# Performance work log

Hardware: AMD Instinct MI355X
Metric: run time of the kernel (lower is better)

## Reference

```python
import jax, jax.numpy as jnp
import numpy as np

S, H = 8192, 2048


def setup_inputs() -> dict:
    key = jax.random.key(0)
    k1, k2, k3, k4, k5 = jax.random.split(key, 5)
    encoder_outputs = jax.random.normal(k1, (S, 1, H), dtype=jnp.float32)
    hidden = jax.random.normal(k2, (H,), dtype=jnp.float32)
    # nn.Linear(2H, H): weight [H, 2H], bias [H]
    lim = 1.0 / np.sqrt(2 * H)
    W_att = jax.random.uniform(k3, (H, 2 * H), dtype=jnp.float32, minval=-lim, maxval=lim)
    b_att = jax.random.uniform(k4, (H,), dtype=jnp.float32, minval=-lim, maxval=lim)
    w = jax.random.normal(k5, (1, H), dtype=jnp.float32)
    return {"encoder_outputs": encoder_outputs, "hidden": hidden,
            "W_att": W_att, "b_att": b_att, "w": w}


def reference(encoder_outputs, hidden, W_att, b_att, w):
    # Original loops over source_len: score_i = w . (Linear(cat(hidden, enc_i)))
    # Vectorized: build [S, 2H] once, one GEMM, one dot, one softmax.
    enc = encoder_outputs[:, 0, :]                      # [S, H]
    h = jnp.broadcast_to(hidden[None, :], enc.shape)    # [S, H]
    x = jnp.concatenate([h, enc], axis=1)               # [S, 2H]
    res = x @ W_att.T + b_att                           # [S, H]
    scores = res @ w[0]                                 # [S]
    attn = jax.nn.softmax(scores, axis=0)               # softmax over source_len
    return attn[None, None, :]                          # [1, 1, S]
```

## Files before the change

kernel.cpp:

```cpp
#include <hip/hip_runtime.h>
#include <math.h>

#define SS 8192
#define HH 2048

__global__ void colsum_kernel(const float* __restrict__ W,
                              const float* __restrict__ w,
                              float* __restrict__ v2) {
    const int t       = threadIdx.x;
    const int colBase = blockIdx.x * 1024;
    const int row0    = blockIdx.y * 32;
    const float4* base =
        (const float4*)(W + (size_t)row0 * (2 * HH) + HH + colBase) + t;
    float4 acc = {0.f, 0.f, 0.f, 0.f};
#pragma unroll
    for (int j = 0; j < 32; ++j) {
        float4 a = base[(size_t)j * ((2 * HH) / 4)];
        float wj = w[row0 + j];
        acc.x += wj * a.x; acc.y += wj * a.y;
        acc.z += wj * a.z; acc.w += wj * a.w;
    }
    float* dst = v2 + colBase + t * 4;
    atomicAdd(dst + 0, acc.x);
    atomicAdd(dst + 1, acc.y);
    atomicAdd(dst + 2, acc.z);
    atomicAdd(dst + 3, acc.w);
}

__global__ __launch_bounds__(256) void rowdot_kernel(
    const float* __restrict__ enc,
    const float* __restrict__ v2,
    float* __restrict__ sc)
{
    const int wave = threadIdx.x >> 6;
    const int lane = threadIdx.x & 63;
    const float4* v = (const float4*)v2;
    float4 vf[8];
#pragma unroll
    for (int i = 0; i < 8; ++i) vf[i] = v[lane + i * 64];

    const int row_base = blockIdx.x * 8 + wave * 2;
#pragma unroll
    for (int rr = 0; rr < 2; ++rr) {
        const int row = row_base + rr;
        const float4* e = (const float4*)(enc + (size_t)row * HH);
        float acc = 0.0f;
#pragma unroll
        for (int i = 0; i < 8; ++i) {
            float4 a = e[lane + i * 64];
            acc += a.x * vf[i].x + a.y * vf[i].y
                 + a.z * vf[i].z + a.w * vf[i].w;
        }
#pragma unroll
        for (int off = 32; off > 0; off >>= 1)
            acc += __shfl_down(acc, off);
        if (lane == 0) sc[row] = acc;
    }
}

__global__ __launch_bounds__(256) void softmax_kernel(
    const float* __restrict__ sc,
    float* __restrict__ out)
{
    __shared__ float red[4];
    const int t    = threadIdx.x;
    const int lane = t & 63;
    const int wid  = t >> 6;

    float vals[32];
    float m = -INFINITY;
#pragma unroll
    for (int i = 0; i < 32; ++i) {
        vals[i] = sc[t + i * 256];
        m = fmaxf(m, vals[i]);
    }
#pragma unroll
    for (int off = 1; off < 64; off <<= 1)
        m = fmaxf(m, __shfl_xor(m, off));
    if (lane == 0) red[wid] = m;
    __syncthreads();
    m = fmaxf(fmaxf(red[0], red[1]), fmaxf(red[2], red[3]));

    float s = 0.0f;
#pragma unroll
    for (int i = 0; i < 32; ++i)
        s += __expf(vals[i] - m);
#pragma unroll
    for (int off = 1; off < 64; off <<= 1)
        s += __shfl_xor(s, off);
    __syncthreads();
    if (lane == 0) red[wid] = s;
    __syncthreads();
    const float inv = 1.0f / (red[0] + red[1] + red[2] + red[3]);

    if (t < 16) {
        const int e = blockIdx.x * 16 + t;
        out[e] = __expf(sc[e] - m) * inv;
    }
}

extern "C" void kernel_launch(void* const* d_in, const int* in_sizes, int n_in,
                              void* d_out, int out_size, void* d_ws, size_t ws_size,
                              hipStream_t stream) {
    const float* enc   = (const float*)d_in[0];
    const float* W_att = (const float*)d_in[2];
    const float* w     = (const float*)d_in[4];

    float* out = (float*)d_out;
    float* v2  = (float*)d_ws;
    float* sc  = v2 + HH;

    hipMemsetAsync(v2, 0, HH * sizeof(float), stream);
    hipLaunchKernelGGL(colsum_kernel,  dim3(2, 64), dim3(256), 0, stream,
                       W_att, w, v2);
    hipLaunchKernelGGL(rowdot_kernel,  dim3(1024), dim3(256), 0, stream,
                       enc, v2, sc);
    hipLaunchKernelGGL(softmax_kernel, dim3(512),  dim3(256), 0, stream,
                       sc, out);
}
```

Baseline: 126.0 us.

## Fuse colsum, rowdot and softmax into one persistent kernel with grid barriers

Replaces the memset plus three kernel launches with a single persistent kernel of 256 blocks that synchronises phases through a software grid barrier built on device-scope atomics. The w·W column-sum vector now lives in a device global, and block 0 re-zeroes it at the end so the memset is no longer needed. The aim is to remove launch gaps and inter-kernel drain. The cost is that all blocks must be co-resident for the barrier to work, and blocks spin-wait on atomics in between phases.

```diff
diff --git a/kernel.cpp b/kernel.cpp
--- a/kernel.cpp
+++ b/kernel.cpp
@@ -3,99 +3,138 @@
 
 #define SS 8192
 #define HH 2048
+#define NBLK 256
+#define NTHR 512
 
-__global__ void colsum_kernel(const float* __restrict__ W,
-                              const float* __restrict__ w,
-                              float* __restrict__ v2) {
-    const int t       = threadIdx.x;
-    const int colBase = blockIdx.x * 1024;
-    const int row0    = blockIdx.y * 32;
-    const float4* base =
-        (const float4*)(W + (size_t)row0 * (2 * HH) + HH + colBase) + t;
-    float4 acc = {0.f, 0.f, 0.f, 0.f};
-#pragma unroll
-    for (int j = 0; j < 32; ++j) {
-        float4 a = base[(size_t)j * ((2 * HH) / 4)];
-        float wj = w[row0 + j];
-        acc.x += wj * a.x; acc.y += wj * a.y;
-        acc.z += wj * a.z; acc.w += wj * a.w;
+__device__ unsigned g_count = 0;
+__device__ unsigned g_gen   = 0;
+__device__ __align__(16) float g_v2[HH];
+
+__device__ __forceinline__ void grid_barrier() {
+    __syncthreads();
+    if (threadIdx.x == 0) {
+        __threadfence();
+        unsigned my  = __hip_atomic_load(&g_gen, __ATOMIC_RELAXED,
+                                         __HIP_MEMORY_SCOPE_AGENT);
+        unsigned old = __hip_atomic_fetch_add(&g_count, 1u, __ATOMIC_ACQ_REL,
+                                              __HIP_MEMORY_SCOPE_AGENT);
+        if (old == NBLK - 1u) {
+            __hip_atomic_store(&g_count, 0u, __ATOMIC_RELAXED,
+                               __HIP_MEMORY_SCOPE_AGENT);
+            __hip_atomic_fetch_add(&g_gen, 1u, __ATOMIC_RELEASE,
+                                   __HIP_MEMORY_SCOPE_AGENT);
+        } else {
+            while (__hip_atomic_load(&g_gen, __ATOMIC_ACQUIRE,
+                                     __HIP_MEMORY_SCOPE_AGENT) == my)
+                __builtin_amdgcn_s_sleep(2);
+        }
+        __threadfence();
     }
-    float* dst = v2 + colBase + t * 4;
-    atomicAdd(dst + 0, acc.x);
-    atomicAdd(dst + 1, acc.y);
-    atomicAdd(dst + 2, acc.z);
-    atomicAdd(dst + 3, acc.w);
+    __syncthreads();
 }
 
-__global__ __launch_bounds__(256) void rowdot_kernel(
+__global__ __launch_bounds__(NTHR, 2) void fused_kernel(
     const float* __restrict__ enc,
-    const float* __restrict__ v2,
+    const float* __restrict__ W,
+    const float* __restrict__ w,
+    float* __restrict__ out,
     float* __restrict__ sc)
 {
-    const int wave = threadIdx.x >> 6;
-    const int lane = threadIdx.x & 63;
-    const float4* v = (const float4*)v2;
-    float4 vf[8];
+    const int b = blockIdx.x;
+    const int t = threadIdx.x;
+
+    {
+        const int row0 = b * 8;
+        const float4* base =
+            (const float4*)(W + (size_t)row0 * (2 * HH) + HH) + t;
+        float4 acc = {0.f, 0.f, 0.f, 0.f};
 #pragma unroll
-    for (int i = 0; i < 8; ++i) vf[i] = v[lane + i * 64];
+        for (int j = 0; j < 8; ++j) {
+            float4 a = base[(size_t)j * ((2 * HH) / 4)];
+            float wj = w[row0 + j];
+            acc.x += wj * a.x; acc.y += wj * a.y;
+            acc.z += wj * a.z; acc.w += wj * a.w;
+        }
+        float* dst = g_v2 + t * 4;
+        atomicAdd(dst + 0, acc.x);
+        atomicAdd(dst + 1, acc.y);
+        atomicAdd(dst + 2, acc.z);
+        atomicAdd(dst + 3, acc.w);
+    }
 
-    const int row_base = blockIdx.x * 8 + wave * 2;
+    grid_barrier();
+
+    {
+        const int wave = t >> 6;
+        const int lane = t & 63;
+        const float4* v = (const float4*)g_v2;
+        float4 vf[8];
 #pragma unroll
-    for (int rr = 0; rr < 2; ++rr) {
-        const int row = row_base + rr;
-        const float4* e = (const float4*)(enc + (size_t)row * HH);
-        float acc = 0.0f;
+        for (int i = 0; i < 8; ++i) vf[i] = v[lane + i * 64];
+
+        const int row_base = b * 32 + wave * 4;
 #pragma unroll
-        for (int i = 0; i < 8; ++i) {
-            float4 a = e[lane + i * 64];
-            acc += a.x * vf[i].x + a.y * vf[i].y
-                 + a.z * vf[i].z + a.w * vf[i].w;
+        for (int rr = 0; rr < 4; ++rr) {
+            const int row = row_base + rr;
+            const float4* e = (const float4*)(enc + (size_t)row * HH);
+            float acc = 0.0f;
+#pragma unroll
+            for (int i = 0; i < 8; ++i) {
+                float4 a = e[lane + i * 64];
+                acc += a.x * vf[i].x + a.y * vf[i].y
+                     + a.z * vf[i].z + a.w * vf[i].w;
+            }
+#pragma unroll
+            for (int off = 32; off > 0; off >>= 1)
+                acc += __shfl_down(acc, off);
+            if (lane == 0) sc[row] = acc;
+        }
+    }
+
+    grid_barrier();
+
+    {
+        __shared__ float red[8];
+        const int lane = t & 63;
+        const int wid  = t >> 6;
+
+        float vals[16];
+        float m = -INFINITY;
+#pragma unroll
+        for (int i = 0; i < 16; ++i) {
+            vals[i] = sc[t + i * 512];
+            m = fmaxf(m, vals[i]);
         }
 #pragma unroll
-        for (int off = 32; off > 0; off >>= 1)
-            acc += __shfl_down(acc, off);
-        if (lane == 0) sc[row] = acc;
-    }
-}
+        for (int off = 1; off < 64; off <<= 1)
+            m = fmaxf(m, __shfl_xor(m, off));
+        if (lane == 0) red[wid] = m;
+        __syncthreads();
+#pragma unroll
+        for (int k = 0; k < 8; ++k) m = fmaxf(m, red[k]);
 
-__global__ __launch_bounds__(256) void softmax_kernel(
-    const float* __restrict__ sc,
-    float* __restrict__ out)
-{
-    __shared__ float red[4];
-    const int t    = threadIdx.x;
-    const int lane = t & 63;
-    const int wid  = t >> 6;
+        float s = 0.0f;
+#pragma unroll
+        for (int i = 0; i < 16; ++i)
+            s += __expf(vals[i] - m);
+#pragma unroll
+        for (int off = 1; off < 64; off <<= 1)
+            s += __shfl_xor(s, off);
+        __syncthreads();
+        if (lane == 0) red[wid] = s;
+        __syncthreads();
+        float ss = 0.0f;
+#pragma unroll
+        for (int k = 0; k < 8; ++k) ss += red[k];
+        const float inv = 1.0f / ss;
 
-    float vals[32];
-    float m = -INFINITY;
-#pragma unroll
-    for (int i = 0; i < 32; ++i) {
-        vals[i] = sc[t + i * 256];
-        m = fmaxf(m, vals[i]);
-    }
-#pragma unroll
-    for (int off = 1; off < 64; off <<= 1)
-        m = fmaxf(m, __shfl_xor(m, off));
-    if (lane == 0) red[wid] = m;
-    __syncthreads();
-    m = fmaxf(fmaxf(red[0], red[1]), fmaxf(red[2], red[3]));
+        if (t < 32) {
+            const int e = b * 32 + t;
+            out[e] = __expf(sc[e] - m) * inv;
+        }
 
-    float s = 0.0f;
-#pragma unroll
-    for (int i = 0; i < 32; ++i)
-        s += __expf(vals[i] - m);
-#pragma unroll
-    for (int off = 1; off < 64; off <<= 1)
-        s += __shfl_xor(s, off);
-    __syncthreads();
-    if (lane == 0) red[wid] = s;
-    __syncthreads();
-    const float inv = 1.0f / (red[0] + red[1] + red[2] + red[3]);
-
-    if (t < 16) {
-        const int e = blockIdx.x * 16 + t;
-        out[e] = __expf(sc[e] - m) * inv;
+        if (b == 0)
+            ((float4*)g_v2)[t] = make_float4(0.f, 0.f, 0.f, 0.f);
     }
 }
 
@@ -107,14 +146,8 @@
     const float* w     = (const float*)d_in[4];
 
     float* out = (float*)d_out;
-    float* v2  = (float*)d_ws;
-    float* sc  = v2 + HH;
+    float* sc  = (float*)d_ws;
 
-    hipMemsetAsync(v2, 0, HH * sizeof(float), stream);
-    hipLaunchKernelGGL(colsum_kernel,  dim3(2, 64), dim3(256), 0, stream,
-                       W_att, w, v2);
-    hipLaunchKernelGGL(rowdot_kernel,  dim3(1024), dim3(256), 0, stream,
-                       enc, v2, sc);
-    hipLaunchKernelGGL(softmax_kernel, dim3(512),  dim3(256), 0, stream,
-                       sc, out);
+    hipLaunchKernelGGL(fused_kernel, dim3(NBLK), dim3(NTHR), 0, stream,
+                       enc, W_att, w, out, sc);
 }
```

Measured after the change: 223.4 us. +77.2%, slower.

## Drop memset, split atomic partials, stage v2 in LDS, one row per wave

Applied to the files above, without the earlier changes.

Removes the hipMemsetAsync launch by keeping partial column sums in device globals that the softmax kernel zeroes for the next call. colsum now uses twice as many blocks, each with 16 rows preloaded into registers, and spreads its atomics over 4 partial buffers to reduce contention. rowdot uses 512-thread blocks with one row per wave, issues the enc loads before summing the partial buffers into shared memory, then reads v2 from LDS. It depends on the globals being zero at the first call and on the cleanup in softmax running in stream order.

```diff
diff --git a/kernel.cpp b/kernel.cpp
--- a/kernel.cpp
+++ b/kernel.cpp
@@ -3,75 +3,97 @@
 
 #define SS 8192
 #define HH 2048
+#define NP 4
 
-__global__ void colsum_kernel(const float* __restrict__ W,
-                              const float* __restrict__ w,
-                              float* __restrict__ v2) {
+__device__ float g_v2p[NP][HH];
+__device__ float g_sc[SS];
+
+__global__ __launch_bounds__(256) void colsum_kernel(
+    const float* __restrict__ W,
+    const float* __restrict__ w)
+{
     const int t       = threadIdx.x;
     const int colBase = blockIdx.x * 1024;
-    const int row0    = blockIdx.y * 32;
+    const int row0    = blockIdx.y * 16;
     const float4* base =
         (const float4*)(W + (size_t)row0 * (2 * HH) + HH + colBase) + t;
+
+    float4 wv[16];
+#pragma unroll
+    for (int j = 0; j < 16; ++j)
+        wv[j] = base[(size_t)j * ((2 * HH) / 4)];
+
     float4 acc = {0.f, 0.f, 0.f, 0.f};
 #pragma unroll
-    for (int j = 0; j < 32; ++j) {
-        float4 a = base[(size_t)j * ((2 * HH) / 4)];
-        float wj = w[row0 + j];
-        acc.x += wj * a.x; acc.y += wj * a.y;
-        acc.z += wj * a.z; acc.w += wj * a.w;
+    for (int j = 0; j < 16; ++j) {
+        const float wj = w[row0 + j];
+        acc.x += wj * wv[j].x; acc.y += wj * wv[j].y;
+        acc.z += wj * wv[j].z; acc.w += wj * wv[j].w;
     }
-    float* dst = v2 + colBase + t * 4;
+    float* dst = &g_v2p[blockIdx.y & (NP - 1)][colBase + t * 4];
     atomicAdd(dst + 0, acc.x);
     atomicAdd(dst + 1, acc.y);
     atomicAdd(dst + 2, acc.z);
     atomicAdd(dst + 3, acc.w);
 }
 
-__global__ __launch_bounds__(256) void rowdot_kernel(
-    const float* __restrict__ enc,
-    const float* __restrict__ v2,
-    float* __restrict__ sc)
+__global__ __launch_bounds__(512) void rowdot_kernel(
+    const float* __restrict__ enc)
 {
-    const int wave = threadIdx.x >> 6;
-    const int lane = threadIdx.x & 63;
-    const float4* v = (const float4*)v2;
-    float4 vf[8];
+    __shared__ float v2s[HH];
+    const int t    = threadIdx.x;
+    const int wave = t >> 6;
+    const int lane = t & 63;
+    const int row  = blockIdx.x * 8 + wave;
+
+    const float4* e = (const float4*)(enc + (size_t)row * HH);
+    float4 er[8];
 #pragma unroll
-    for (int i = 0; i < 8; ++i) vf[i] = v[lane + i * 64];
+    for (int i = 0; i < 8; ++i)
+        er[i] = e[lane + i * 64];
 
-    const int row_base = blockIdx.x * 8 + wave * 2;
+    {
+        float4 s4 = {0.f, 0.f, 0.f, 0.f};
 #pragma unroll
-    for (int rr = 0; rr < 2; ++rr) {
-        const int row = row_base + rr;
-        const float4* e = (const float4*)(enc + (size_t)row * HH);
-        float acc = 0.0f;
+        for (int p = 0; p < NP; ++p) {
+            float4 a = ((const float4*)g_v2p[p])[t];
+            s4.x += a.x; s4.y += a.y; s4.z += a.z; s4.w += a.w;
+        }
+        ((float4*)v2s)[t] = s4;
+    }
+    __syncthreads();
+
+    const float4* v4 = (const float4*)v2s;
+    float acc = 0.0f;
 #pragma unroll
-        for (int i = 0; i < 8; ++i) {
-            float4 a = e[lane + i * 64];
-            acc += a.x * vf[i].x + a.y * vf[i].y
-                 + a.z * vf[i].z + a.w * vf[i].w;
-        }
+    for (int i = 0; i < 8; ++i) {
+        const float4 vf = v4[lane + i * 64];
+        acc += er[i].x * vf.x + er[i].y * vf.y
+             + er[i].z * vf.z + er[i].w * vf.w;
+    }
 #pragma unroll
-        for (int off = 32; off > 0; off >>= 1)
-            acc += __shfl_down(acc, off);
-        if (lane == 0) sc[row] = acc;
-    }
+    for (int off = 32; off > 0; off >>= 1)
+        acc += __shfl_down(acc, off);
+    if (lane == 0) g_sc[row] = acc;
 }
 
 __global__ __launch_bounds__(256) void softmax_kernel(
-    const float* __restrict__ sc,
     float* __restrict__ out)
 {
     __shared__ float red[4];
     const int t    = threadIdx.x;
     const int lane = t & 63;
     const int wid  = t >> 6;
+    const int b    = blockIdx.x;
+
+    if (b < 8)
+        ((float4*)g_v2p)[b * 256 + t] = make_float4(0.f, 0.f, 0.f, 0.f);
 
     float vals[32];
     float m = -INFINITY;
 #pragma unroll
     for (int i = 0; i < 32; ++i) {
-        vals[i] = sc[t + i * 256];
+        vals[i] = g_sc[t + i * 256];
         m = fmaxf(m, vals[i]);
     }
 #pragma unroll
@@ -94,8 +116,8 @@
     const float inv = 1.0f / (red[0] + red[1] + red[2] + red[3]);
 
     if (t < 16) {
-        const int e = blockIdx.x * 16 + t;
-        out[e] = __expf(sc[e] - m) * inv;
+        const int e = b * 16 + t;
+        out[e] = __expf(g_sc[e] - m) * inv;
     }
 }
 
@@ -107,14 +129,11 @@
     const float* w     = (const float*)d_in[4];
 
     float* out = (float*)d_out;
-    float* v2  = (float*)d_ws;
-    float* sc  = v2 + HH;
 
-    hipMemsetAsync(v2, 0, HH * sizeof(float), stream);
-    hipLaunchKernelGGL(colsum_kernel,  dim3(2, 64), dim3(256), 0, stream,
-                       W_att, w, v2);
-    hipLaunchKernelGGL(rowdot_kernel,  dim3(1024), dim3(256), 0, stream,
-                       enc, v2, sc);
-    hipLaunchKernelGGL(softmax_kernel, dim3(512),  dim3(256), 0, stream,
-                       sc, out);
+    hipLaunchKernelGGL(colsum_kernel,  dim3(2, 128), dim3(256), 0, stream,
+                       W_att, w);
+    hipLaunchKernelGGL(rowdot_kernel,  dim3(1024),   dim3(512), 0, stream,
+                       enc);
+    hipLaunchKernelGGL(softmax_kernel, dim3(512),    dim3(256), 0, stream,
+                       out);
 }
```

Measured after the change: 121.6 us. 1.04x faster.
